# Kernel optimization log

Hardware: AMD Instinct MI355X
Metric: run time of the kernel (lower is better)

The kernel has to match this reference:

```python
import jax, jax.numpy as jnp
import numpy as np

N_NODES = 50000
N_EDGES = 600000
N_LABEL = 200000
IN_CH = 128
OUT_CH = 128
K_HOPS = 2


def setup_inputs() -> dict:
    key = jax.random.key(0)
    ks = jax.random.split(key, 9)
    x = jax.random.normal(ks[0], (N_NODES, IN_CH), dtype=jnp.float32)
    edge_index = jax.random.randint(ks[1], (2, N_EDGES), 0, N_NODES)
    edge_label_index = jax.random.randint(ks[2], (2, N_LABEL), 0, N_NODES)
    conv_weight = jax.random.normal(ks[3], (OUT_CH, IN_CH), dtype=jnp.float32) * 0.05
    conv_bias = jax.random.normal(ks[4], (OUT_CH,), dtype=jnp.float32) * 0.05
    w1 = jax.random.normal(ks[5], (OUT_CH // 2, OUT_CH), dtype=jnp.float32) * 0.05
    b1 = jax.random.normal(ks[6], (OUT_CH // 2,), dtype=jnp.float32) * 0.05
    w2 = jax.random.normal(ks[7], (1, OUT_CH // 2), dtype=jnp.float32) * 0.05
    b2 = jax.random.normal(ks[8], (1,), dtype=jnp.float32) * 0.05
    return {"x": x, "edge_index": edge_index, "edge_label_index": edge_label_index,
            "conv_weight": conv_weight, "conv_bias": conv_bias,
            "w1": w1, "b1": b1, "w2": w2, "b2": b2}


def reference(x, edge_index, edge_label_index, conv_weight, conv_bias, w1, b1, w2, b2):
    n = x.shape[0]
    # gcn_norm with self-loops: A_hat = D^{-1/2} (A + I) D^{-1/2}
    loop = jnp.arange(n, dtype=edge_index.dtype)
    src = jnp.concatenate([edge_index[0], loop])  # message sources
    dst = jnp.concatenate([edge_index[1], loop])  # aggregation targets
    deg = jax.ops.segment_sum(jnp.ones_like(dst, dtype=x.dtype), dst, num_segments=n)
    dinv = jnp.where(deg > 0, jax.lax.rsqrt(deg), 0.0)
    w = dinv[src] * dinv[dst]  # [E+N] edge weights

    # K-hop propagation: h <- A_hat h, repeated K times (SGConv)
    h = x
    for _ in range(K_HOPS):
        h = jax.ops.segment_sum(h[src] * w[:, None], dst, num_segments=n)
    z = h @ conv_weight.T + conv_bias  # [N, out_channels]

    # decode: gather endpoint embeddings, multiply, tiny MLP (dropout inactive at eval)
    s = z[edge_label_index[0]] * z[edge_label_index[1]]  # [E_label, out]
    h1 = jax.nn.relu(s @ w1.T + b1)
    r = (h1 @ w2.T + b2).sum(axis=-1)  # [E_label]
    return r
```

## Files before the change

### kernel.cpp

```cpp
#include <hip/hip_runtime.h>

#define N_CH 128

typedef _Float16 half8  __attribute__((ext_vector_type(8)));
typedef _Float16 half4v __attribute__((ext_vector_type(4)));
typedef float    floatx4 __attribute__((ext_vector_type(4)));


__global__ void k_prep(int* __restrict__ cnt,
                       const float* __restrict__ W,  _Float16* __restrict__ wh,
                       const float* __restrict__ W1, _Float16* __restrict__ w1h,
                       int n) {
    int i = blockIdx.x * blockDim.x + threadIdx.x;
    if (i < n) cnt[i] = 0;
    int nw4  = N_CH * N_CH / 4;
    int nw14 = 64 * N_CH / 4;
    if (i < nw4) {
        float4 v = ((const float4*)W)[i];
        half4v o;
        o[0] = (_Float16)v.x; o[1] = (_Float16)v.y; o[2] = (_Float16)v.z; o[3] = (_Float16)v.w;
        ((half4v*)wh)[i] = o;
    } else if (i < nw4 + nw14) {
        int j = i - nw4;
        float4 v = ((const float4*)W1)[j];
        half4v o;
        o[0] = (_Float16)v.x; o[1] = (_Float16)v.y; o[2] = (_Float16)v.z; o[3] = (_Float16)v.w;
        ((half4v*)w1h)[j] = o;
    }
}


__global__ void k_count(const int* __restrict__ dst, int* __restrict__ cnt, int E) {
    int e = blockIdx.x * blockDim.x + threadIdx.x;
    if (e < E) atomicAdd(&cnt[dst[e]], 1);
}

__global__ __launch_bounds__(1024) void k_scan1(const int* __restrict__ cnt,
                                                int* __restrict__ offs,
                                                int* __restrict__ bsum, int n) {
    __shared__ int ssum[16];
    int tid = threadIdx.x;
    int lane = tid & 63, wid = tid >> 6;
    int i = blockIdx.x * 1024 + tid;
    int v = (i < n) ? ((cnt[i] + 7) & ~7) : 0;
    int x = v;
    #pragma unroll
    for (int off = 1; off < 64; off <<= 1) {
        int y = __shfl_up(x, off, 64);
        if (lane >= off) x += y;
    }
    if (lane == 63) ssum[wid] = x;
    __syncthreads();
    if (wid == 0 && lane < 16) {
        int s = ssum[lane];
        #pragma unroll
        for (int off = 1; off < 16; off <<= 1) {
            int y = __shfl_up(s, off, 64);
            if (lane >= off) s += y;
        }
        ssum[lane] = s;
    }
    __syncthreads();
    int waveoff = (wid > 0) ? ssum[wid - 1] : 0;
    int incl = x + waveoff;
    if (i < n) offs[i] = incl - v;
    if (tid == 1023) bsum[blockIdx.x] = incl;
}

__global__ __launch_bounds__(256) void k_scan3(const int* __restrict__ cnt,
                                               int* __restrict__ offs,
                                               const int* __restrict__ bsum,
                                               int* __restrict__ cur,
                                               float* __restrict__ dinv,
                                               unsigned short* __restrict__ csr,
                                               int n, int nb) {
    __shared__ int sbb[64];
    int tid = threadIdx.x;
    if (tid < 64) {
        int v = (tid < nb) ? bsum[tid] : 0;
        int x = v;
        #pragma unroll
        for (int off = 1; off < 64; off <<= 1) {
            int y = __shfl_up(x, off, 64);
            if (tid >= off) x += y;
        }
        sbb[tid] = x - v;
    }
    __syncthreads();
    int i = blockIdx.x * blockDim.x + tid;
    if (i < n) {
        int o = offs[i] + sbb[i >> 10];
        offs[i] = o;
        cur[i]  = o;
        int c = cnt[i];
        dinv[i] = rsqrtf((float)(c + 1));
        int cp = (c + 7) & ~7;
        unsigned short zn = (unsigned short)n;
        for (int j = c; j < cp; ++j) csr[o + j] = zn;
    }
}

__global__ void k_fill(const int* __restrict__ src, const int* __restrict__ dst,
                       int* __restrict__ cur, unsigned short* __restrict__ csr, int E) {
    int e = blockIdx.x * blockDim.x + threadIdx.x;
    if (e < E) {
        int p = atomicAdd(&cur[dst[e]], 1);
        csr[p] = (unsigned short)src[e];
    }
}


__global__ void k_scale(const float* __restrict__ x, const float* __restrict__ dinv,
                        _Float16* __restrict__ u0, _Float16* __restrict__ u1, int n) {
    int i = blockIdx.x * blockDim.x + threadIdx.x;
    int nx4 = n * (N_CH / 4);
    if (i < nx4) {
        float d = dinv[i >> 5];
        float4 v = ((const float4*)x)[i];
        half4v o;
        o[0] = (_Float16)(d * v.x); o[1] = (_Float16)(d * v.y);
        o[2] = (_Float16)(d * v.z); o[3] = (_Float16)(d * v.w);
        ((half4v*)u0)[i] = o;
    } else if (i < nx4 + 64) {
        int j = i - nx4;
        half4v zz; zz[0] = (_Float16)0.f; zz[1] = (_Float16)0.f; zz[2] = (_Float16)0.f; zz[3] = (_Float16)0.f;
        _Float16* dst16 = (j < 32) ? u0 : u1;
        ((half4v*)(dst16 + (size_t)n * N_CH))[j & 31] = zz;
    }
}


__global__ __launch_bounds__(256) void k_hop16(const _Float16* __restrict__ hin,
                                               _Float16* __restrict__ hout,
                                               const int* __restrict__ offs,
                                               const int* __restrict__ cnt,
                                               const float* __restrict__ dinv,
                                               const unsigned short* __restrict__ csr,
                                               int n, int squared) {
    int tid  = threadIdx.x;
    int node = blockIdx.x * 16 + (tid >> 4);
    int c16  = tid & 15;
    if (node >= n) return;
    float di = dinv[node];
    float sc = squared ? di * di : di;
    int s0 = offs[node];
    int cp = (cnt[node] + 7) & ~7;
    const uint4* qlst = (const uint4*)(csr + s0);
    half8 self = ((const half8*)(hin + (size_t)node * N_CH))[c16];
    float acc[8];
    #pragma unroll
    for (int j = 0; j < 8; ++j) acc[j] = (float)self[j];
    int nq = cp >> 3;
    uint4 pk;
    if (nq > 0) pk = qlst[0];
    for (int q = 0; q < nq; ++q) {
        uint4 cpk = pk;
        if (q + 1 < nq) pk = qlst[q + 1];
        int idx[8];
        idx[0] = cpk.x & 0xFFFF; idx[1] = cpk.x >> 16;
        idx[2] = cpk.y & 0xFFFF; idx[3] = cpk.y >> 16;
        idx[4] = cpk.z & 0xFFFF; idx[5] = cpk.z >> 16;
        idx[6] = cpk.w & 0xFFFF; idx[7] = cpk.w >> 16;
        half8 u[8];
        #pragma unroll
        for (int i = 0; i < 8; ++i)
            u[i] = ((const half8*)(hin + (size_t)idx[i] * N_CH))[c16];
        #pragma unroll
        for (int i = 0; i < 8; ++i)
            #pragma unroll
            for (int j = 0; j < 8; ++j) acc[j] += (float)u[i][j];
    }
    half8 o;
    #pragma unroll
    for (int j = 0; j < 8; ++j) o[j] = (_Float16)(sc * acc[j]);
    ((half8*)(hout + (size_t)node * N_CH))[c16] = o;
}


__global__ __launch_bounds__(256) void k_zlin_mfma(const _Float16* __restrict__ h,
                                                   const _Float16* __restrict__ wh,
                                                   const float* __restrict__ bc,
                                                   _Float16* __restrict__ z, int n) {
    __shared__ half8 wls[128 * 16];
    int tid = threadIdx.x;
    int lane = tid & 63, w = tid >> 6;
    int quad = lane >> 4, m16 = lane & 15;
    int nb = blockIdx.x * 64;
    #pragma unroll
    for (int i = 0; i < 8; ++i) {
        int g = tid + 256 * i;
        int r = g >> 4, c = g & 15;
        wls[r * 16 + (c ^ (r & 15))] = ((const half8*)wh)[g];
    }
    int arow = nb + w * 16 + m16;
    const half8* hrow = (const half8*)(h + (size_t)arow * N_CH);
    half8 a[4];
    #pragma unroll
    for (int kk = 0; kk < 4; ++kk) a[kk] = hrow[kk * 4 + quad];
    __syncthreads();
    int outnode0 = nb + w * 16 + quad * 4;
    #pragma unroll
    for (int jt = 0; jt < 8; ++jt) {
        floatx4 acc = {0.f, 0.f, 0.f, 0.f};
        #pragma unroll
        for (int kk = 0; kk < 4; ++kk) {
            int r = jt * 16 + m16;
            half8 bfr = wls[r * 16 + ((kk * 4 + quad) ^ m16)];
            acc = __builtin_amdgcn_mfma_f32_16x16x32_f16(a[kk], bfr, acc, 0, 0, 0);
        }
        int j = jt * 16 + m16;
        float bias = bc[j];
        #pragma unroll
        for (int reg = 0; reg < 4; ++reg) {
            int node = outnode0 + reg;
            if (node < n) z[(size_t)node * N_CH + j] = (_Float16)(acc[reg] + bias);
        }
    }
}


__global__ __launch_bounds__(256) void k_decode_mfma(const _Float16* __restrict__ z,
        const int* __restrict__ ai, const int* __restrict__ bi,
        const _Float16* __restrict__ w1h, const float* __restrict__ b1,
        const float* __restrict__ w2, const float* __restrict__ b2,
        float* __restrict__ out, int m) {
    __shared__ half8 w1ls[64 * 16];
    __shared__ half8 sls[64 * 16];
    int tid = threadIdx.x;
    int lane = tid & 63, w = tid >> 6;
    int quad = lane >> 4, m16 = lane & 15;
    int pbase = blockIdx.x * 64;
    #pragma unroll
    for (int i = 0; i < 4; ++i) {
        int g = tid + 256 * i;
        int r = g >> 4, c = g & 15;
        w1ls[r * 16 + (c ^ (r & 15))] = ((const half8*)w1h)[g];
    }
    int pidx = pbase + w * 16 + m16;
    if (pidx >= m) pidx = m - 1;
    int idxa = ai[pidx];
    int idxb = bi[pidx];
    int ia[4], ib[4];
    #pragma unroll
    for (int it = 0; it < 4; ++it) {
        int p = it * 4 + quad;
        ia[it] = __shfl(idxa, p, 64);
        ib[it] = __shfl(idxb, p, 64);
    }
    half8 za[4], zb[4];
    #pragma unroll
    for (int it = 0; it < 4; ++it) {
        za[it] = ((const half8*)(z + (size_t)ia[it] * N_CH))[m16];
        zb[it] = ((const half8*)(z + (size_t)ib[it] * N_CH))[m16];
    }
    #pragma unroll
    for (int it = 0; it < 4; ++it) {
        half8 s8 = za[it] * zb[it];
        int pp = w * 16 + it * 4 + quad;
        sls[pp * 16 + (m16 ^ (pp & 15))] = s8;
    }
    __syncthreads();
    half8 a[4];
    #pragma unroll
    for (int kk = 0; kk < 4; ++kk)
        a[kk] = sls[(w * 16 + m16) * 16 + ((kk * 4 + quad) ^ m16)];
    float rsum[4] = {0.f, 0.f, 0.f, 0.f};
    #pragma unroll
    for (int jt = 0; jt < 4; ++jt) {
        floatx4 acc = {0.f, 0.f, 0.f, 0.f};
        #pragma unroll
        for (int kk = 0; kk < 4; ++kk) {
            int r = jt * 16 + m16;
            half8 bfr = w1ls[r * 16 + ((kk * 4 + quad) ^ m16)];
            acc = __builtin_amdgcn_mfma_f32_16x16x32_f16(a[kk], bfr, acc, 0, 0, 0);
        }
        int j = jt * 16 + m16;
        float b1j = b1[j], w2j = w2[j];
        #pragma unroll
        for (int reg = 0; reg < 4; ++reg) {
            float v = fmaxf(acc[reg] + b1j, 0.f) * w2j;
            v += __shfl_xor(v, 1, 64);
            v += __shfl_xor(v, 2, 64);
            v += __shfl_xor(v, 4, 64);
            v += __shfl_xor(v, 8, 64);
            rsum[reg] += v;
        }
    }
    if (m16 == 0) {
        float bb = b2[0];
        #pragma unroll
        for (int reg = 0; reg < 4; ++reg) {
            int gp = pbase + w * 16 + quad * 4 + reg;
            if (gp < m) out[gp] = rsum[reg] + bb;
        }
    }
}


extern "C" void kernel_launch(void* const* d_in, const int* in_sizes, int n_in,
                              void* d_out, int out_size, void* d_ws, size_t ws_size,
                              hipStream_t stream) {
    const float* x   = (const float*)d_in[0];
    const int*   ei  = (const int*)d_in[1];
    const int*   eli = (const int*)d_in[2];
    const float* W   = (const float*)d_in[3];
    const float* bc  = (const float*)d_in[4];
    const float* W1  = (const float*)d_in[5];
    const float* b1  = (const float*)d_in[6];
    const float* w2  = (const float*)d_in[7];
    const float* b2  = (const float*)d_in[8];
    float* out = (float*)d_out;

    const int N = in_sizes[0] / N_CH;
    const int E = in_sizes[1] / 2;
    const int M = in_sizes[2] / 2;

    const int* src = ei;
    const int* dst = ei + E;
    const int* ai  = eli;
    const int* bi  = eli + M;

    _Float16* hb0 = (_Float16*)d_ws;
    _Float16* hb1 = hb0 + (size_t)(N + 1) * N_CH;
    _Float16* wh  = hb1 + (size_t)(N + 1) * N_CH;
    _Float16* w1h = wh + 16384;
    unsigned short* csr = (unsigned short*)(w1h + 8192);
    int*   cnt  = (int*)(csr + (size_t)E + 8 * (size_t)N);
    int*   off  = cnt + N;
    int*   cur  = off + N;
    float* dnv  = (float*)(cur + N);
    int*   bsum = (int*)(dnv + N);

    int nb = (N + 1023) / 1024;
    k_prep<<<(N + 255) / 256, 256, 0, stream>>>(cnt, W, wh, W1, w1h, N);
    k_count<<<(E + 255) / 256, 256, 0, stream>>>(dst, cnt, E);
    k_scan1<<<nb, 1024, 0, stream>>>(cnt, off, bsum, N);
    k_scan3<<<(N + 255) / 256, 256, 0, stream>>>(cnt, off, bsum, cur, dnv, csr, N, nb);
    k_fill<<<(E + 255) / 256, 256, 0, stream>>>(src, dst, cur, csr, E);
    int sc_work = N * (N_CH / 4) + 64;
    k_scale<<<(sc_work + 255) / 256, 256, 0, stream>>>(x, dnv, hb0, hb1, N);

    int hop_blocks = (N + 15) / 16;
    k_hop16<<<hop_blocks, 256, 0, stream>>>(hb0, hb1, off, cnt, dnv, csr, N, 1);
    k_hop16<<<hop_blocks, 256, 0, stream>>>(hb1, hb0, off, cnt, dnv, csr, N, 0);

    k_zlin_mfma<<<(N + 63) / 64, 256, 0, stream>>>(hb0, wh, bc, hb1, N);

    k_decode_mfma<<<(M + 63) / 64, 256, 0, stream>>>(hb1, ai, bi, w1h, b1, w2, b2, out, M);
}
```

Baseline: 233.6 us.

## Split hop gather across channel halves and neighbor rows with wavefront reduction

Each wavefront now handles one node for one half of the channels (two grid passes), with its 8 row groups processing different neighbors of each 8-neighbor packet in parallel and combining partial sums via cross-lane shuffles. This raises the number of independent gathers in flight per node and shortens the serial per-node loop, targeting latency in the gather-bound SpMM hops. It adds shuffle reductions, padded dummy-row loads, duplicated index reads across the two passes, and uses nontemporal stores for the output.

```diff
diff --git a/kernel.cpp b/kernel.cpp
--- a/kernel.cpp
+++ b/kernel.cpp
@@ -130,50 +130,66 @@
 }
 
 
-__global__ __launch_bounds__(256) void k_hop16(const _Float16* __restrict__ hin,
-                                               _Float16* __restrict__ hout,
-                                               const int* __restrict__ offs,
-                                               const int* __restrict__ cnt,
-                                               const float* __restrict__ dinv,
-                                               const unsigned short* __restrict__ csr,
-                                               int n, int squared) {
-    int tid  = threadIdx.x;
-    int node = blockIdx.x * 16 + (tid >> 4);
-    int c16  = tid & 15;
+__global__ __launch_bounds__(256) void k_hop_split(const _Float16* __restrict__ hin,
+                                                   _Float16* __restrict__ hout,
+                                                   const int* __restrict__ offs,
+                                                   const int* __restrict__ cnt,
+                                                   const float* __restrict__ dinv,
+                                                   const unsigned short* __restrict__ csr,
+                                                   int n, int squared, int nblk) {
+    int pass = (blockIdx.x >= nblk) ? 1 : 0;
+    int bid  = blockIdx.x - pass * nblk;
+    int node = bid * 4 + (threadIdx.x >> 6);
     if (node >= n) return;
+    int lane = threadIdx.x & 63;
+    int r = lane >> 3;
+    int c = lane & 7;
+    int cbase = pass * 8 + c;
     float di = dinv[node];
     float sc = squared ? di * di : di;
     int s0 = offs[node];
-    int cp = (cnt[node] + 7) & ~7;
+    int nq = ((cnt[node] + 7) & ~7) >> 3;
     const uint4* qlst = (const uint4*)(csr + s0);
-    half8 self = ((const half8*)(hin + (size_t)node * N_CH))[c16];
     float acc[8];
     #pragma unroll
-    for (int j = 0; j < 8; ++j) acc[j] = (float)self[j];
-    int nq = cp >> 3;
-    uint4 pk;
-    if (nq > 0) pk = qlst[0];
-    for (int q = 0; q < nq; ++q) {
-        uint4 cpk = pk;
-        if (q + 1 < nq) pk = qlst[q + 1];
-        int idx[8];
-        idx[0] = cpk.x & 0xFFFF; idx[1] = cpk.x >> 16;
-        idx[2] = cpk.y & 0xFFFF; idx[3] = cpk.y >> 16;
-        idx[4] = cpk.z & 0xFFFF; idx[5] = cpk.z >> 16;
-        idx[6] = cpk.w & 0xFFFF; idx[7] = cpk.w >> 16;
-        half8 u[8];
-        #pragma unroll
-        for (int i = 0; i < 8; ++i)
-            u[i] = ((const half8*)(hin + (size_t)idx[i] * N_CH))[c16];
-        #pragma unroll
-        for (int i = 0; i < 8; ++i)
+    for (int j = 0; j < 8; ++j) acc[j] = 0.0f;
+    for (int q0 = 0; q0 < nq; q0 += 4) {
+        int idx[4];
+        #pragma unroll
+        for (int t = 0; t < 4; ++t) {
+            int q = q0 + t;
+            int id = n;
+            if (q < nq) {
+                uint4 pk = qlst[q];
+                unsigned long long lo = ((unsigned long long)pk.y << 32) | pk.x;
+                unsigned long long hi = ((unsigned long long)pk.w << 32) | pk.z;
+                unsigned long long sel = (r < 4) ? lo : hi;
+                id = (int)((sel >> ((r & 3) * 16)) & 0xFFFF);
+            }
+            idx[t] = id;
+        }
+        half8 u[4];
+        #pragma unroll
+        for (int t = 0; t < 4; ++t)
+            u[t] = ((const half8*)(hin + (size_t)idx[t] * N_CH))[cbase];
+        #pragma unroll
+        for (int t = 0; t < 4; ++t)
             #pragma unroll
-            for (int j = 0; j < 8; ++j) acc[j] += (float)u[i][j];
-    }
-    half8 o;
-    #pragma unroll
-    for (int j = 0; j < 8; ++j) o[j] = (_Float16)(sc * acc[j]);
-    ((half8*)(hout + (size_t)node * N_CH))[c16] = o;
+            for (int j = 0; j < 8; ++j) acc[j] += (float)u[t][j];
+    }
+    #pragma unroll
+    for (int j = 0; j < 8; ++j) {
+        acc[j] += __shfl_xor(acc[j], 8, 64);
+        acc[j] += __shfl_xor(acc[j], 16, 64);
+        acc[j] += __shfl_xor(acc[j], 32, 64);
+    }
+    if (r == 0) {
+        half8 self = ((const half8*)(hin + (size_t)node * N_CH))[cbase];
+        half8 o;
+        #pragma unroll
+        for (int j = 0; j < 8; ++j) o[j] = (_Float16)(sc * ((float)self[j] + acc[j]));
+        __builtin_nontemporal_store(o, ((half8*)(hout + (size_t)node * N_CH)) + cbase);
+    }
 }
 
 
@@ -340,9 +356,9 @@
     int sc_work = N * (N_CH / 4) + 64;
     k_scale<<<(sc_work + 255) / 256, 256, 0, stream>>>(x, dnv, hb0, hb1, N);
 
-    int hop_blocks = (N + 15) / 16;
-    k_hop16<<<hop_blocks, 256, 0, stream>>>(hb0, hb1, off, cnt, dnv, csr, N, 1);
-    k_hop16<<<hop_blocks, 256, 0, stream>>>(hb1, hb0, off, cnt, dnv, csr, N, 0);
+    int nblk = (N + 3) / 4;
+    k_hop_split<<<2 * nblk, 256, 0, stream>>>(hb0, hb1, off, cnt, dnv, csr, N, 1, nblk);
+    k_hop_split<<<2 * nblk, 256, 0, stream>>>(hb1, hb0, off, cnt, dnv, csr, N, 0, nblk);
 
     k_zlin_mfma<<<(N + 63) / 64, 256, 0, stream>>>(hb0, wh, bc, hb1, N);
 
```

After: 268.9 us. +15.1%, slower.

## Split hop gather into two channel-half passes with eight lanes per node

Applied to the files above, without the earlier changes.

The propagation kernel now gives each node eight lanes covering one 64-channel half of its fp16 row. The grid doubles so the first set of blocks handles channels 0-63 and the second set handles 64-127. This narrows the working set of gathered rows per pass, so neighbour data is more likely to stay in L2/MALL, and each lane's gather becomes a 128-byte segment. The cost is reading the CSR index lists twice and dropping the software prefetch of the next packed index word.

```diff
diff --git a/kernel.cpp b/kernel.cpp
--- a/kernel.cpp
+++ b/kernel.cpp
@@ -130,41 +130,41 @@
 }
 
 
-__global__ __launch_bounds__(256) void k_hop16(const _Float16* __restrict__ hin,
-                                               _Float16* __restrict__ hout,
-                                               const int* __restrict__ offs,
-                                               const int* __restrict__ cnt,
-                                               const float* __restrict__ dinv,
-                                               const unsigned short* __restrict__ csr,
-                                               int n, int squared) {
+__global__ __launch_bounds__(256) void k_hop8(const _Float16* __restrict__ hin,
+                                              _Float16* __restrict__ hout,
+                                              const int* __restrict__ offs,
+                                              const int* __restrict__ cnt,
+                                              const float* __restrict__ dinv,
+                                              const unsigned short* __restrict__ csr,
+                                              int n, int squared, int nblk) {
+    int pass = (blockIdx.x >= nblk) ? 1 : 0;
+    int bid  = blockIdx.x - pass * nblk;
     int tid  = threadIdx.x;
-    int node = blockIdx.x * 16 + (tid >> 4);
-    int c16  = tid & 15;
+    int node = bid * 32 + (tid >> 3);
+    int c8   = tid & 7;
     if (node >= n) return;
+    int cbase = pass * 8 + c8;
     float di = dinv[node];
     float sc = squared ? di * di : di;
     int s0 = offs[node];
     int cp = (cnt[node] + 7) & ~7;
     const uint4* qlst = (const uint4*)(csr + s0);
-    half8 self = ((const half8*)(hin + (size_t)node * N_CH))[c16];
+    half8 self = ((const half8*)(hin + (size_t)node * N_CH))[cbase];
     float acc[8];
     #pragma unroll
     for (int j = 0; j < 8; ++j) acc[j] = (float)self[j];
     int nq = cp >> 3;
-    uint4 pk;
-    if (nq > 0) pk = qlst[0];
     for (int q = 0; q < nq; ++q) {
-        uint4 cpk = pk;
-        if (q + 1 < nq) pk = qlst[q + 1];
+        uint4 pk = qlst[q];
         int idx[8];
-        idx[0] = cpk.x & 0xFFFF; idx[1] = cpk.x >> 16;
-        idx[2] = cpk.y & 0xFFFF; idx[3] = cpk.y >> 16;
-        idx[4] = cpk.z & 0xFFFF; idx[5] = cpk.z >> 16;
-        idx[6] = cpk.w & 0xFFFF; idx[7] = cpk.w >> 16;
+        idx[0] = pk.x & 0xFFFF; idx[1] = pk.x >> 16;
+        idx[2] = pk.y & 0xFFFF; idx[3] = pk.y >> 16;
+        idx[4] = pk.z & 0xFFFF; idx[5] = pk.z >> 16;
+        idx[6] = pk.w & 0xFFFF; idx[7] = pk.w >> 16;
         half8 u[8];
         #pragma unroll
         for (int i = 0; i < 8; ++i)
-            u[i] = ((const half8*)(hin + (size_t)idx[i] * N_CH))[c16];
+            u[i] = ((const half8*)(hin + (size_t)idx[i] * N_CH))[cbase];
         #pragma unroll
         for (int i = 0; i < 8; ++i)
             #pragma unroll
@@ -173,7 +173,7 @@
     half8 o;
     #pragma unroll
     for (int j = 0; j < 8; ++j) o[j] = (_Float16)(sc * acc[j]);
-    ((half8*)(hout + (size_t)node * N_CH))[c16] = o;
+    ((half8*)(hout + (size_t)node * N_CH))[cbase] = o;
 }
 
 
@@ -340,9 +340,9 @@
     int sc_work = N * (N_CH / 4) + 64;
     k_scale<<<(sc_work + 255) / 256, 256, 0, stream>>>(x, dnv, hb0, hb1, N);
 
-    int hop_blocks = (N + 15) / 16;
-    k_hop16<<<hop_blocks, 256, 0, stream>>>(hb0, hb1, off, cnt, dnv, csr, N, 1);
-    k_hop16<<<hop_blocks, 256, 0, stream>>>(hb1, hb0, off, cnt, dnv, csr, N, 0);
+    int nblk = (N + 31) / 32;
+    k_hop8<<<2 * nblk, 256, 0, stream>>>(hb0, hb1, off, cnt, dnv, csr, N, 1, nblk);
+    k_hop8<<<2 * nblk, 256, 0, stream>>>(hb1, hb0, off, cnt, dnv, csr, N, 0, nblk);
 
     k_zlin_mfma<<<(N + 63) / 64, 256, 0, stream>>>(hb0, wh, bc, hb1, N);
 
```

Measured after the change: 224.1 us, median of 2. -4.1%, faster.
